# Kernel tuning notes

Measured on AMD Instinct MI355X. Metric: run time of the kernel, lower is better.

## Reference

```python
import jax, jax.numpy as jnp
import numpy as np

N, E, D, H = 50000, 500000, 128, 4
C = D // H
EPS = 1e-5


def _layer_norm(x, g, b):
    mu = jnp.mean(x, axis=-1, keepdims=True)
    var = jnp.mean((x - mu) ** 2, axis=-1, keepdims=True)
    return (x - mu) * jax.lax.rsqrt(var + EPS) * g + b


def setup_inputs() -> dict:
    key = jax.random.key(0)
    ks = jax.random.split(key, 20)
    f = lambda i, shape: jax.random.normal(ks[i], shape, dtype=jnp.float32) * 0.05
    return {
        "x": f(0, (N, D)),
        "edge_index": jax.random.randint(ks[1], (2, E), 0, N),
        "w_gcn": f(2, (D, D)), "b_gcn": f(3, (D,)),
        "wq": f(4, (D, D)), "bq": f(5, (D,)),
        "wk": f(6, (D, D)), "bk": f(7, (D,)),
        "wv": f(8, (D, D)), "bv": f(9, (D,)),
        "w_skip": f(10, (D, D)), "b_skip": f(11, (D,)),
        "w_beta": f(12, (3 * D, 1)),
        "g1": jnp.ones((D,), jnp.float32), "b1": jnp.zeros((D,), jnp.float32),
        "g2": jnp.ones((D,), jnp.float32), "b2": jnp.zeros((D,), jnp.float32),
        "w_rel": f(13, (D, 2 * D)), "w_root": f(14, (2 * D, D)),
        "local_w": jnp.ones((1,), jnp.float32), "global_w": jnp.ones((1,), jnp.float32),
    }


def reference(x, edge_index, w_gcn, b_gcn, wq, bq, wk, bk, wv, bv,
              w_skip, b_skip, w_beta, g1, b1, g2, b2, w_rel, w_root,
              local_w, global_w):
    src, dst = edge_index[0], edge_index[1]

    # ---- GCNConv (add_self_loops=False, symmetric norm) ----
    xw = x @ w_gcn                                   # [N, D]
    deg = jax.ops.segment_sum(jnp.ones((E,), x.dtype), dst, num_segments=N)
    dinv = jnp.where(deg > 0, jax.lax.rsqrt(jnp.maximum(deg, 1.0)), 0.0)
    coef = dinv[src] * dinv[dst]                     # [E]
    local_out = jax.ops.segment_sum(coef[:, None] * xw[src], dst, num_segments=N) + b_gcn

    # ---- TransformerConv (heads=4, concat=True, beta=True) ----
    q = (x @ wq + bq).reshape(N, H, C)
    k = (x @ wk + bk).reshape(N, H, C)
    v = (x @ wv + bv).reshape(N, H, C)
    alpha = jnp.sum(q[dst] * k[src], axis=-1) / jnp.sqrt(jnp.float32(C))  # [E, H]
    m = jax.ops.segment_max(alpha, dst, num_segments=N)
    m = jnp.where(jnp.isfinite(m), m, 0.0)
    a = jnp.exp(alpha - m[dst])
    s = jax.ops.segment_sum(a, dst, num_segments=N)
    attn = a / jnp.maximum(s[dst], 1e-16)            # [E, H] segment softmax over in-edges
    agg = jax.ops.segment_sum(attn[..., None] * v[src], dst, num_segments=N)
    out_g = agg.reshape(N, D)
    x_r = x @ w_skip + b_skip
    beta = jax.nn.sigmoid(jnp.concatenate([out_g, x_r, out_g - x_r], axis=-1) @ w_beta)
    global_out = beta * x_r + (1.0 - beta) * out_g

    # ---- combine + norm + FFN ----
    h = local_w * local_out + global_w * global_out
    h = _layer_norm(h + h, g1, b1)
    out = jax.nn.relu(h @ w_rel) @ w_root
    out = _layer_norm(out + h, g2, b2)
    return out
```

## Files before the change

### kernel.cpp

```cpp
#include <hip/hip_runtime.h>
#include <math.h>

#define D 128
#define EPSV 1e-5f

typedef unsigned short ushort_t;
typedef __attribute__((ext_vector_type(8))) short short8v;
typedef __attribute__((ext_vector_type(4))) float f32x4;

__device__ __forceinline__ float bf2f(unsigned u) {
    return __uint_as_float(u << 16);
}
__device__ __forceinline__ ushort_t f2bf(float f) {
    unsigned u = __float_as_uint(f);
    unsigned r = (u + 0x7fffu + ((u >> 16) & 1u)) >> 16;
    return (ushort_t)r;
}
__device__ __forceinline__ float bfp(uint4 v, int i) {
    unsigned w = (&v.x)[i >> 1];
    return bf2f((i & 1) ? (w >> 16) : (w & 0xffffu));
}

__global__ __launch_bounds__(256)
void proj_gemm(const float* __restrict__ x,
               const ushort_t* __restrict__ Bt,
               const float* __restrict__ bias,
               ushort_t* __restrict__ pack, ushort_t* __restrict__ qb,
               ushort_t* __restrict__ xrb, int M)
{
    __shared__ ushort_t Cs[128 * 136];
    const int tid = threadIdx.x, lane = tid & 63, wid = tid >> 6;
    const int wr = wid >> 1, wc = wid & 1;
    const int R0 = blockIdx.x * 128;
    const int cbeg = blockIdx.y ? 3 : 0;
    const int cend = blockIdx.y ? 5 : 3;

    short8v av[4][4];
    #pragma unroll
    for (int r = 0; r < 4; ++r) {
        int gr = R0 + wr * 64 + r * 16 + (lane & 15);
        if (gr >= M) gr = M - 1;
        const float* xrow = x + (size_t)gr * 128 + (lane >> 4) * 8;
        #pragma unroll
        for (int ks = 0; ks < 4; ++ks) {
            float4 lo = *reinterpret_cast<const float4*>(xrow + ks * 32);
            float4 hi = *reinterpret_cast<const float4*>(xrow + ks * 32 + 4);
            short8v a;
            a[0] = (short)f2bf(lo.x); a[1] = (short)f2bf(lo.y);
            a[2] = (short)f2bf(lo.z); a[3] = (short)f2bf(lo.w);
            a[4] = (short)f2bf(hi.x); a[5] = (short)f2bf(hi.y);
            a[6] = (short)f2bf(hi.z); a[7] = (short)f2bf(hi.w);
            av[r][ks] = a;
        }
    }

    for (int ct = cbeg; ct < cend; ++ct) {
        f32x4 acc[4][4] = {};
        #pragma unroll
        for (int ks = 0; ks < 4; ++ks) {
            short8v bv[4];
            #pragma unroll
            for (int c = 0; c < 4; ++c) {
                int col = ct * 128 + wc * 64 + c * 16 + (lane & 15);
                bv[c] = *reinterpret_cast<const short8v*>(
                    &Bt[(size_t)col * 128 + ks * 32 + (lane >> 4) * 8]);
            }
            #pragma unroll
            for (int r = 0; r < 4; ++r)
                #pragma unroll
                for (int c = 0; c < 4; ++c)
                    acc[r][c] = __builtin_amdgcn_mfma_f32_16x16x32_bf16(av[r][ks], bv[c], acc[r][c], 0, 0, 0);
        }
        __syncthreads();
        #pragma unroll
        for (int r = 0; r < 4; ++r) {
            int rowb = wr * 64 + r * 16 + (lane >> 4) * 4;
            #pragma unroll
            for (int i = 0; i < 4; ++i)
                #pragma unroll
                for (int c = 0; c < 4; ++c) {
                    int col = wc * 64 + c * 16 + (lane & 15);
                    Cs[(rowb + i) * 136 + col] = f2bf(acc[r][c][i] + bias[ct * 128 + col]);
                }
        }
        __syncthreads();
        #pragma unroll
        for (int it = 0; it < 8; ++it) {
            int linear = tid + it * 256;
            int row = linear >> 4, ch = linear & 15;
            int gr = R0 + row;
            if (gr < M) {
                uint4 v = *reinterpret_cast<const uint4*>(&Cs[row * 136 + ch * 8]);
                ushort_t* dst;
                if (ct == 0)      dst = pack + (size_t)gr * 384 + 256;
                else if (ct == 1) dst = qb   + (size_t)gr * 128;
                else if (ct == 2) dst = pack + (size_t)gr * 384;
                else if (ct == 3) dst = pack + (size_t)gr * 384 + 128;
                else              dst = xrb  + (size_t)gr * 128;
                *reinterpret_cast<uint4*>(dst + ch * 8) = v;
            }
        }
    }
}

__device__ __forceinline__ int swz(int ch, int row) {
    return (ch & 24) | ((ch ^ row) & 7);
}

__global__ __launch_bounds__(256)
void ffn_fused(const ushort_t* __restrict__ hlnb,
               const ushort_t* __restrict__ wt_rel,
               const ushort_t* __restrict__ wt_root,
               const float* __restrict__ g2, const float* __restrict__ b2,
               float* __restrict__ outf, int M)
{
    __shared__ float smem[128 * 130];
    ushort_t* Hs = (ushort_t*)smem;
    const int tid = threadIdx.x, lane = tid & 63, wid = tid >> 6;
    const int wr = wid >> 1, wc = wid & 1;
    const int R0 = blockIdx.x * 128;

    short8v av[4][4];
    #pragma unroll
    for (int r = 0; r < 4; ++r) {
        int gr = R0 + wr * 64 + r * 16 + (lane & 15);
        if (gr >= M) gr = M - 1;
        #pragma unroll
        for (int ks = 0; ks < 4; ++ks)
            av[r][ks] = *reinterpret_cast<const short8v*>(
                &hlnb[(size_t)gr * 128 + ks * 32 + (lane >> 4) * 8]);
    }
    for (int ct = 0; ct < 2; ++ct) {
        f32x4 acc[4][4] = {};
        #pragma unroll
        for (int ks = 0; ks < 4; ++ks) {
            short8v bv[4];
            #pragma unroll
            for (int c = 0; c < 4; ++c) {
                int col = ct * 128 + wc * 64 + c * 16 + (lane & 15);
                bv[c] = *reinterpret_cast<const short8v*>(
                    &wt_rel[(size_t)col * 128 + ks * 32 + (lane >> 4) * 8]);
            }
            #pragma unroll
            for (int r = 0; r < 4; ++r)
                #pragma unroll
                for (int c = 0; c < 4; ++c)
                    acc[r][c] = __builtin_amdgcn_mfma_f32_16x16x32_bf16(av[r][ks], bv[c], acc[r][c], 0, 0, 0);
        }
        #pragma unroll
        for (int r = 0; r < 4; ++r) {
            int rowb = wr * 64 + r * 16 + (lane >> 4) * 4;
            #pragma unroll
            for (int i = 0; i < 4; ++i)
                #pragma unroll
                for (int c = 0; c < 4; ++c) {
                    int row = rowb + i;
                    int col = ct * 128 + wc * 64 + c * 16 + (lane & 15);
                    int ch = col >> 3, el = col & 7;
                    Hs[row * 256 + swz(ch, row) * 8 + el] = f2bf(fmaxf(acc[r][c][i], 0.f));
                }
        }
    }
    __syncthreads();

    f32x4 acc2[4][4] = {};
    #pragma unroll
    for (int ks = 0; ks < 8; ++ks) {
        short8v a2[4], bv[4];
        #pragma unroll
        for (int r = 0; r < 4; ++r) {
            int row = wr * 64 + r * 16 + (lane & 15);
            int ch = ks * 4 + (lane >> 4);
            a2[r] = *reinterpret_cast<const short8v*>(&Hs[row * 256 + swz(ch, row) * 8]);
        }
        #pragma unroll
        for (int c = 0; c < 4; ++c) {
            int col = wc * 64 + c * 16 + (lane & 15);
            bv[c] = *reinterpret_cast<const short8v*>(
                &wt_root[(size_t)col * 256 + ks * 32 + (lane >> 4) * 8]);
        }
        #pragma unroll
        for (int r = 0; r < 4; ++r)
            #pragma unroll
            for (int c = 0; c < 4; ++c)
                acc2[r][c] = __builtin_amdgcn_mfma_f32_16x16x32_bf16(a2[r], bv[c], acc2[r][c], 0, 0, 0);
    }
    __syncthreads();

    float* Cs = smem;
    #pragma unroll
    for (int r = 0; r < 4; ++r) {
        int rowb = wr * 64 + r * 16 + (lane >> 4) * 4;
        #pragma unroll
        for (int i = 0; i < 4; ++i)
            #pragma unroll
            for (int c = 0; c < 4; ++c)
                Cs[(rowb + i) * 130 + wc * 64 + c * 16 + (lane & 15)] = acc2[r][c][i];
    }
    __syncthreads();

    const float ga = g2[lane * 2], gb = g2[lane * 2 + 1];
    const float ba = b2[lane * 2], bb2 = b2[lane * 2 + 1];
    for (int rr = 0; rr < 32; ++rr) {
        int row = wid * 32 + rr;
        int gr = R0 + row;
        if (gr >= M) break;
        unsigned hu = *reinterpret_cast<const unsigned*>(&hlnb[(size_t)gr * 128 + lane * 2]);
        float t0 = Cs[row * 130 + lane * 2]     + bf2f(hu & 0xffffu);
        float t1 = Cs[row * 130 + lane * 2 + 1] + bf2f(hu >> 16);
        float ssum = t0 + t1;
        #pragma unroll
        for (int off = 1; off <= 32; off <<= 1) ssum += __shfl_xor(ssum, off);
        float mu = ssum * (1.f / 128.f);
        float dv0 = t0 - mu, dv1 = t1 - mu;
        float vsum = dv0 * dv0 + dv1 * dv1;
        #pragma unroll
        for (int off = 1; off <= 32; off <<= 1) vsum += __shfl_xor(vsum, off);
        float rs = rsqrtf(vsum * (1.f / 128.f) + EPSV);
        float2 o = make_float2(dv0 * rs * ga + ba, dv1 * rs * gb + bb2);
        *reinterpret_cast<float2*>(&outf[(size_t)gr * 128 + lane * 2]) = o;
    }
}

__global__ void pack_weights_kernel(const float* __restrict__ wg, const float* __restrict__ wq,
                                    const float* __restrict__ wk, const float* __restrict__ wv,
                                    const float* __restrict__ wsk,
                                    const float* __restrict__ bq, const float* __restrict__ bk,
                                    const float* __restrict__ bv, const float* __restrict__ bsk,
                                    const float* __restrict__ wrel, const float* __restrict__ wroot,
                                    ushort_t* __restrict__ wt_all, ushort_t* __restrict__ wt_rel,
                                    ushort_t* __restrict__ wt_root, float* __restrict__ bias_all)
{
    int i = blockIdx.x * 256 + threadIdx.x;
    if (i < 640 * 128) {
        int n = i >> 7, k = i & 127;
        const float* srcs[5] = {wg, wq, wk, wv, wsk};
        wt_all[i] = f2bf(srcs[n >> 7][k * 128 + (n & 127)]);
    } else if (i < 640 * 128 + 256 * 128) {
        int j = i - 640 * 128;
        int n = j >> 7, k = j & 127;
        wt_rel[j] = f2bf(wrel[k * 256 + n]);
    } else if (i < 640 * 128 + 256 * 128 + 128 * 256) {
        int j = i - (640 * 128 + 256 * 128);
        int n = j >> 8, k = j & 255;
        wt_root[j] = f2bf(wroot[k * 128 + n]);
    } else if (i < 640 * 128 + 256 * 128 + 128 * 256 + 640) {
        int n = i - (640 * 128 + 256 * 128 + 128 * 256);
        float b = 0.f;
        if (n >= 128) {
            const float* bs[4] = {bq, bk, bv, bsk};
            b = bs[(n - 128) >> 7][n & 127];
        }
        bias_all[n] = b;
    }
}

__global__ void deg_count_kernel(const int* __restrict__ dst, int* __restrict__ deg, int E)
{
    int e = blockIdx.x * blockDim.x + threadIdx.x;
    if (e < E) atomicAdd(&deg[dst[e]], 1);
}

__global__ __launch_bounds__(256)
void scan1_kernel(const int* __restrict__ deg, int* __restrict__ row_start,
                  int* __restrict__ bsum, int n)
{
    __shared__ int ws[4];
    const int t = threadIdx.x, lane = t & 63, wid = t >> 6;
    const int base = blockIdx.x * 1024 + t * 4;
    int v0 = 0, v1 = 0, v2 = 0, v3 = 0;
    if (base + 3 < n) {
        int4 q = *reinterpret_cast<const int4*>(&deg[base]);
        v0 = q.x; v1 = q.y; v2 = q.z; v3 = q.w;
    } else {
        if (base < n)     v0 = deg[base];
        if (base + 1 < n) v1 = deg[base + 1];
        if (base + 2 < n) v2 = deg[base + 2];
        if (base + 3 < n) v3 = deg[base + 3];
    }
    int tot = v0 + v1 + v2 + v3;
    int inc = tot;
    #pragma unroll
    for (int off = 1; off < 64; off <<= 1) {
        int y = __shfl_up(inc, off);
        if (lane >= off) inc += y;
    }
    if (lane == 63) ws[wid] = inc;
    __syncthreads();
    int woff = 0;
    for (int w = 0; w < wid; ++w) woff += ws[w];
    int excl = woff + inc - tot;
    if (base < n)     row_start[base]     = excl;
    if (base + 1 < n) row_start[base + 1] = excl + v0;
    if (base + 2 < n) row_start[base + 2] = excl + v0 + v1;
    if (base + 3 < n) row_start[base + 3] = excl + v0 + v1 + v2;
    if (t == 0) bsum[blockIdx.x] = ws[0] + ws[1] + ws[2] + ws[3];
}

__global__ __launch_bounds__(256)
void scan2_kernel(int* __restrict__ bsum, int nb)
{
    __shared__ int ws[4];
    const int t = threadIdx.x, lane = t & 63, wid = t >> 6;
    const int base = t * 4;
    int v0 = 0, v1 = 0, v2 = 0, v3 = 0;
    if (base < nb)     v0 = bsum[base];
    if (base + 1 < nb) v1 = bsum[base + 1];
    if (base + 2 < nb) v2 = bsum[base + 2];
    if (base + 3 < nb) v3 = bsum[base + 3];
    int tot = v0 + v1 + v2 + v3;
    int inc = tot;
    #pragma unroll
    for (int off = 1; off < 64; off <<= 1) {
        int y = __shfl_up(inc, off);
        if (lane >= off) inc += y;
    }
    if (lane == 63) ws[wid] = inc;
    __syncthreads();
    int woff = 0;
    for (int w = 0; w < wid; ++w) woff += ws[w];
    int excl = woff + inc - tot;
    if (base < nb)     bsum[base]     = excl;
    if (base + 1 < nb) bsum[base + 1] = excl + v0;
    if (base + 2 < nb) bsum[base + 2] = excl + v0 + v1;
    if (base + 3 < nb) bsum[base + 3] = excl + v0 + v1 + v2;
}

__global__ void scan3_kernel(const int* __restrict__ deg, const int* __restrict__ bsum,
                             int* __restrict__ row_start, int* __restrict__ cursor,
                             float* __restrict__ dinv, int n, int E)
{
    int i = blockIdx.x * blockDim.x + threadIdx.x;
    if (i < n) {
        int rs = row_start[i] + bsum[i >> 10];
        row_start[i] = rs;
        cursor[i] = rs;
        int d = deg[i];
        dinv[i] = (d > 0) ? rsqrtf((float)d) : 0.f;
    }
    if (i == 0) row_start[n] = E;
}

__global__ void fill_kernel(const int* __restrict__ src, const int* __restrict__ dst,
                            int* __restrict__ cursor, int* __restrict__ csr_src, int E)
{
    int e = blockIdx.x * blockDim.x + threadIdx.x;
    if (e < E) {
        int d = dst[e];
        int pos = atomicAdd(&cursor[d], 1);
        csr_src[pos] = src[e];
    }
}

__global__ __launch_bounds__(256)
void edge_fused_kernel(const ushort_t* __restrict__ pack,
                       const ushort_t* __restrict__ qbf,
                       const ushort_t* __restrict__ xrbf,
                       const int* __restrict__ row_start,
                       const int* __restrict__ csr_src,
                       const float* __restrict__ dinv,
                       const float* __restrict__ b_gcn,
                       const float* __restrict__ w_beta,
                       const float* __restrict__ g1, const float* __restrict__ b1,
                       const float* __restrict__ local_w, const float* __restrict__ global_w,
                       ushort_t* __restrict__ hln_bf, int n)
{
    const int wid = threadIdx.x >> 6, lane = threadIdx.x & 63;
    const int node = blockIdx.x * 4 + wid;
    if (node >= n) return;
    const int slot = lane >> 4, li = lane & 15;
    const int d8 = li * 8;

    uint4 qu = *reinterpret_cast<const uint4*>(&qbf[(size_t)node * 128 + d8]);
    float q[8];
    #pragma unroll
    for (int i = 0; i < 8; ++i) q[i] = bfp(qu, i);

    const int e0 = row_start[node], e1 = row_start[node + 1];
    const float dn = dinv[node];
    const float scale = 0.17677669529663687f;

    float s = 0.f, va[8] = {}, ga[8] = {};

    for (int j = e0; j < e1; j += 4) {
        const int je = j + slot;
        const bool act = je < e1;
        const int sidx = act ? csr_src[je] : 0;
        const ushort_t* prow = pack + (size_t)sidx * 384;
        uint4 ku = *reinterpret_cast<const uint4*>(&prow[d8]);
        uint4 vu = *reinterpret_cast<const uint4*>(&prow[128 + d8]);
        uint4 xu = *reinterpret_cast<const uint4*>(&prow[256 + d8]);
        float p = 0.f;
        #pragma unroll
        for (int i = 0; i < 8; ++i) p = fmaf(q[i], bfp(ku, i), p);
        p += __shfl_xor(p, 1);
        p += __shfl_xor(p, 2);
        float wgt = act ? __expf(p * scale) : 0.f;
        float c   = act ? dn * dinv[sidx] : 0.f;
        s += wgt;
        #pragma unroll
        for (int i = 0; i < 8; ++i) {
            va[i] = fmaf(wgt, bfp(vu, i), va[i]);
            ga[i] = fmaf(c,   bfp(xu, i), ga[i]);
        }
    }
    #pragma unroll
    for (int off = 16; off <= 32; off <<= 1) {
        s += __shfl_xor(s, off);
        #pragma unroll
        for (int i = 0; i < 8; ++i) {
            va[i] += __shfl_xor(va[i], off);
            ga[i] += __shfl_xor(ga[i], off);
        }
    }
    const float denom = fmaxf(s, 1e-16f);

    uint4 xru = *reinterpret_cast<const uint4*>(&xrbf[(size_t)node * 128 + d8]);
    float t[8];
    float part = 0.f;
    #pragma unroll
    for (int i = 0; i < 8; ++i) {
        float og = va[i] / denom;
        float xr = bfp(xru, i);
        float lo = ga[i] + b_gcn[d8 + i];
        part += og * w_beta[d8 + i] + xr * w_beta[128 + d8 + i]
              + (og - xr) * w_beta[256 + d8 + i];
        t[i] = lo;
        va[i] = og; ga[i] = xr;
    }
    #pragma unroll
    for (int off = 1; off <= 32; off <<= 1) part += __shfl_xor(part, off);
    const float beta = 1.f / (1.f + __expf(-part * 0.25f));

    const float lw = local_w[0], gw = global_w[0];
    float ssum = 0.f;
    #pragma unroll
    for (int i = 0; i < 8; ++i) {
        float go = beta * ga[i] + (1.f - beta) * va[i];
        t[i] = 2.f * (lw * t[i] + gw * go);
        ssum += t[i];
    }
    #pragma unroll
    for (int off = 1; off <= 32; off <<= 1) ssum += __shfl_xor(ssum, off);
    const float mu = ssum * (1.f / 512.f);
    float vsum = 0.f;
    #pragma unroll
    for (int i = 0; i < 8; ++i) { float d = t[i] - mu; vsum += d * d; }
    #pragma unroll
    for (int off = 1; off <= 32; off <<= 1) vsum += __shfl_xor(vsum, off);
    const float rs = rsqrtf(vsum * (1.f / 512.f) + EPSV);

    if (slot == 0) {
        uint4 o;
        #pragma unroll
        for (int i = 0; i < 4; ++i) {
            float o0 = (t[2*i]   - mu) * rs * g1[d8 + 2*i]   + b1[d8 + 2*i];
            float o1 = (t[2*i+1] - mu) * rs * g1[d8 + 2*i+1] + b1[d8 + 2*i+1];
            (&o.x)[i] = (unsigned)f2bf(o0) | ((unsigned)f2bf(o1) << 16);
        }
        *reinterpret_cast<uint4*>(&hln_bf[(size_t)node * 128 + d8]) = o;
    }
}

extern "C" void kernel_launch(void* const* d_in, const int* in_sizes, int n_in,
                              void* d_out, int out_size, void* d_ws, size_t ws_size,
                              hipStream_t stream)
{
    const float* x      = (const float*)d_in[0];
    const int*   ei     = (const int*)d_in[1];
    const float* w_gcn  = (const float*)d_in[2];
    const float* b_gcn  = (const float*)d_in[3];
    const float* wq     = (const float*)d_in[4];
    const float* bq     = (const float*)d_in[5];
    const float* wk     = (const float*)d_in[6];
    const float* bk     = (const float*)d_in[7];
    const float* wv     = (const float*)d_in[8];
    const float* bv     = (const float*)d_in[9];
    const float* w_skip = (const float*)d_in[10];
    const float* b_skip = (const float*)d_in[11];
    const float* w_beta = (const float*)d_in[12];
    const float* g1     = (const float*)d_in[13];
    const float* b1     = (const float*)d_in[14];
    const float* g2     = (const float*)d_in[15];
    const float* b2     = (const float*)d_in[16];
    const float* w_rel  = (const float*)d_in[17];
    const float* w_root = (const float*)d_in[18];
    const float* lw     = (const float*)d_in[19];
    const float* gw     = (const float*)d_in[20];

    const int N = in_sizes[0] / D;
    const int E = in_sizes[1] / 2;
    const int* src = ei;
    const int* dst = ei + E;

    char* wsb = (char*)d_ws;
    size_t off = 0;
    auto alloc = [&](size_t bytes) -> void* {
        void* p = wsb + off;
        off += (bytes + 255) & ~(size_t)255;
        return p;
    };
    ushort_t* pack_kvx = (ushort_t*)alloc((size_t)N * 384 * 2);
    ushort_t* qb_bf    = (ushort_t*)alloc((size_t)N * 128 * 2);
    ushort_t* xr_bf    = (ushort_t*)alloc((size_t)N * 128 * 2);
    ushort_t* hln_bf   = (ushort_t*)alloc((size_t)N * 128 * 2);
    ushort_t* wt_all   = (ushort_t*)alloc(640 * 128 * 2);
    ushort_t* wt_rel   = (ushort_t*)alloc(256 * 128 * 2);
    ushort_t* wt_root  = (ushort_t*)alloc(128 * 256 * 2);
    float*    bias_all = (float*)alloc(640 * 4);
    int*      deg      = (int*)alloc((size_t)N * 4);
    int*      row_start= (int*)alloc((size_t)(N + 1) * 4);
    int*      cursor   = (int*)alloc((size_t)N * 4);
    int*      csr_src  = (int*)alloc((size_t)E * 4);
    float*    dinv     = (float*)alloc((size_t)N * 4);
    int*      bsum     = (int*)alloc(((size_t)(N + 1023) / 1024) * 4);

    float* out = (float*)d_out;
    const int SB = (N + 1023) / 1024;

    hipMemsetAsync(deg, 0, (size_t)N * sizeof(int), stream);
    deg_count_kernel<<<dim3((E + 255) / 256), dim3(256), 0, stream>>>(dst, deg, E);
    scan1_kernel<<<dim3(SB), dim3(256), 0, stream>>>(deg, row_start, bsum, N);
    scan2_kernel<<<dim3(1), dim3(256), 0, stream>>>(bsum, SB);
    scan3_kernel<<<dim3((N + 255) / 256), dim3(256), 0, stream>>>(
        deg, bsum, row_start, cursor, dinv, N, E);
    fill_kernel<<<dim3((E + 255) / 256), dim3(256), 0, stream>>>(src, dst, cursor, csr_src, E);

    pack_weights_kernel<<<dim3(579), dim3(256), 0, stream>>>(
        w_gcn, wq, wk, wv, w_skip, bq, bk, bv, b_skip, w_rel, w_root,
        wt_all, wt_rel, wt_root, bias_all);

    const int MB = (N + 127) / 128;
    proj_gemm<<<dim3(MB, 2), dim3(256), 0, stream>>>(
        x, wt_all, bias_all, pack_kvx, qb_bf, xr_bf, N);

    edge_fused_kernel<<<dim3((N + 3) / 4), dim3(256), 0, stream>>>(
        pack_kvx, qb_bf, xr_bf, row_start, csr_src, dinv, b_gcn, w_beta,
        g1, b1, lw, gw, hln_bf, N);

    ffn_fused<<<dim3(MB), dim3(256), 0, stream>>>(
        hln_bf, wt_rel, wt_root, g2, b2, out, N);
}
```

Before: 234.3 us.

## Fold key and value projections out of edge gather, aggregate raw features

The key weights are folded into the query side: each node gets a per-head q·Wk vector of 512 values. The key bias is dropped because it only shifts every logit of a destination node by the same amount, which cancels in the softmax. The edge kernel now gathers only bf16 x rows (128 values) instead of K, V and X rows (384 values). It builds per-head attention-weighted sums of x plus the GCN sum, and a new combine kernel applies Wv and Wgcn afterwards through MFMA GEMMs, then does the beta gate and the first LayerNorm. This cuts random gather bytes per edge, at the cost of more per-edge arithmetic and a large intermediate aggregate buffer that must be written and read back.

New measurement: 341.9 us. +45.9%, slower.

```diff
diff --git a/kernel.cpp b/kernel.cpp
--- a/kernel.cpp
+++ b/kernel.cpp
@@ -25,8 +25,10 @@
 void proj_gemm(const float* __restrict__ x,
                const ushort_t* __restrict__ Bt,
                const float* __restrict__ bias,
-               ushort_t* __restrict__ pack, ushort_t* __restrict__ qb,
-               ushort_t* __restrict__ xrb, int M)
+               ushort_t* __restrict__ qtb,
+               ushort_t* __restrict__ xrb,
+               ushort_t* __restrict__ xbf,
+               int M)
 {
     __shared__ ushort_t Cs[128 * 136];
     const int tid = threadIdx.x, lane = tid & 63, wid = tid >> 6;
@@ -54,6 +56,19 @@
         }
     }
 
+    if (blockIdx.y == 0) {
+        #pragma unroll
+        for (int r = 0; r < 4; ++r) {
+            int gr = R0 + wr * 64 + r * 16 + (lane & 15);
+            if (gr < M) {
+                #pragma unroll
+                for (int ks = 0; ks < 4; ++ks)
+                    *reinterpret_cast<short8v*>(
+                        &xbf[(size_t)gr * 128 + ks * 32 + (lane >> 4) * 8]) = av[r][ks];
+            }
+        }
+    }
+
     for (int ct = cbeg; ct < cend; ++ct) {
         f32x4 acc[4][4] = {};
         #pragma unroll
@@ -92,14 +107,247 @@
             if (gr < M) {
                 uint4 v = *reinterpret_cast<const uint4*>(&Cs[row * 136 + ch * 8]);
                 ushort_t* dst;
-                if (ct == 0)      dst = pack + (size_t)gr * 384 + 256;
-                else if (ct == 1) dst = qb   + (size_t)gr * 128;
-                else if (ct == 2) dst = pack + (size_t)gr * 384;
-                else if (ct == 3) dst = pack + (size_t)gr * 384 + 128;
-                else              dst = xrb  + (size_t)gr * 128;
+                if (ct < 4) dst = qtb + (size_t)gr * 512 + ct * 128;
+                else        dst = xrb + (size_t)gr * 128;
                 *reinterpret_cast<uint4*>(dst + ch * 8) = v;
             }
         }
+    }
+}
+
+__global__ __launch_bounds__(256)
+void edge_fused_kernel(const ushort_t* __restrict__ xbf,
+                       const ushort_t* __restrict__ qtb,
+                       const int* __restrict__ row_start,
+                       const int* __restrict__ csr_src,
+                       const float* __restrict__ dinv,
+                       ushort_t* __restrict__ agg,
+                       float* __restrict__ flag,
+                       int n)
+{
+    const int wid = threadIdx.x >> 6, lane = threadIdx.x & 63;
+    const int node = blockIdx.x * 4 + wid;
+    if (node >= n) return;
+    const int slot = lane >> 4, li = lane & 15;
+    const int d8 = li * 8;
+
+    float qf[4][8];
+    #pragma unroll
+    for (int h = 0; h < 4; ++h) {
+        uint4 qu = *reinterpret_cast<const uint4*>(&qtb[(size_t)node * 512 + h * 128 + d8]);
+        #pragma unroll
+        for (int i = 0; i < 8; ++i) qf[h][i] = bfp(qu, i);
+    }
+
+    const int e0 = row_start[node], e1 = row_start[node + 1];
+    const float dn = dinv[node];
+    const float scale = 0.17677669529663687f;
+
+    float sh[4] = {}, va[4][8] = {}, ga[8] = {};
+
+    for (int j = e0; j < e1; j += 4) {
+        const int je = j + slot;
+        const bool act = je < e1;
+        const int sidx = act ? csr_src[je] : 0;
+        uint4 xu = *reinterpret_cast<const uint4*>(&xbf[(size_t)sidx * 128 + d8]);
+        float xv[8];
+        #pragma unroll
+        for (int i = 0; i < 8; ++i) xv[i] = bfp(xu, i);
+        float p[4];
+        #pragma unroll
+        for (int h = 0; h < 4; ++h) {
+            float t = 0.f;
+            #pragma unroll
+            for (int i = 0; i < 8; ++i) t = fmaf(qf[h][i], xv[i], t);
+            t += __shfl_xor(t, 1);
+            t += __shfl_xor(t, 2);
+            t += __shfl_xor(t, 4);
+            t += __shfl_xor(t, 8);
+            p[h] = t;
+        }
+        const float c = act ? dn * dinv[sidx] : 0.f;
+        #pragma unroll
+        for (int h = 0; h < 4; ++h) {
+            float w = act ? __expf(p[h] * scale) : 0.f;
+            sh[h] += w;
+            #pragma unroll
+            for (int i = 0; i < 8; ++i) va[h][i] = fmaf(w, xv[i], va[h][i]);
+        }
+        #pragma unroll
+        for (int i = 0; i < 8; ++i) ga[i] = fmaf(c, xv[i], ga[i]);
+    }
+    #pragma unroll
+    for (int off = 16; off <= 32; off <<= 1) {
+        #pragma unroll
+        for (int h = 0; h < 4; ++h) {
+            sh[h] += __shfl_xor(sh[h], off);
+            #pragma unroll
+            for (int i = 0; i < 8; ++i) va[h][i] += __shfl_xor(va[h][i], off);
+        }
+        #pragma unroll
+        for (int i = 0; i < 8; ++i) ga[i] += __shfl_xor(ga[i], off);
+    }
+
+    if (slot == 0) {
+        #pragma unroll
+        for (int h = 0; h < 4; ++h) {
+            float r = 1.f / fmaxf(sh[h], 1e-16f);
+            uint4 o;
+            #pragma unroll
+            for (int i = 0; i < 4; ++i)
+                (&o.x)[i] = (unsigned)f2bf(va[h][2 * i] * r)
+                          | ((unsigned)f2bf(va[h][2 * i + 1] * r) << 16);
+            *reinterpret_cast<uint4*>(&agg[(size_t)node * 640 + h * 128 + d8]) = o;
+        }
+        uint4 og;
+        #pragma unroll
+        for (int i = 0; i < 4; ++i)
+            (&og.x)[i] = (unsigned)f2bf(ga[2 * i]) | ((unsigned)f2bf(ga[2 * i + 1]) << 16);
+        *reinterpret_cast<uint4*>(&agg[(size_t)node * 640 + 512 + d8]) = og;
+        if (li == 0) flag[node] = (sh[0] > 0.f) ? 1.f : 0.f;
+    }
+}
+
+__global__ __launch_bounds__(256)
+void combine_ln1(const ushort_t* __restrict__ agg,
+                 const ushort_t* __restrict__ wt_vg,
+                 const float* __restrict__ bvv, const float* __restrict__ b_gcn,
+                 const float* __restrict__ flag,
+                 const ushort_t* __restrict__ xrb,
+                 const float* __restrict__ w_beta,
+                 const float* __restrict__ g1, const float* __restrict__ b1,
+                 const float* __restrict__ local_w, const float* __restrict__ global_w,
+                 ushort_t* __restrict__ hln_bf, int M)
+{
+    __shared__ float OgS[128 * 130];
+    __shared__ float LoS[128 * 130];
+    const int tid = threadIdx.x, lane = tid & 63, wid = tid >> 6;
+    const int wr = wid >> 1, wc = wid & 1;
+    const int R0 = blockIdx.x * 128;
+
+    {
+        f32x4 acc[4][4] = {};
+        #pragma unroll
+        for (int hl = 0; hl < 2; ++hl) {
+            const int head = wc * 2 + hl;
+            short8v av[4][4];
+            #pragma unroll
+            for (int r = 0; r < 4; ++r) {
+                int gr = R0 + wr * 64 + r * 16 + (lane & 15);
+                if (gr >= M) gr = M - 1;
+                #pragma unroll
+                for (int ks = 0; ks < 4; ++ks)
+                    av[r][ks] = *reinterpret_cast<const short8v*>(
+                        &agg[(size_t)gr * 640 + head * 128 + ks * 32 + (lane >> 4) * 8]);
+            }
+            #pragma unroll
+            for (int cfl = 0; cfl < 2; ++cfl) {
+                const int cf = hl * 2 + cfl;
+                const int col = wc * 64 + cf * 16 + (lane & 15);
+                #pragma unroll
+                for (int ks = 0; ks < 4; ++ks) {
+                    short8v bfrag = *reinterpret_cast<const short8v*>(
+                        &wt_vg[(size_t)col * 128 + ks * 32 + (lane >> 4) * 8]);
+                    #pragma unroll
+                    for (int r = 0; r < 4; ++r)
+                        acc[r][cf] = __builtin_amdgcn_mfma_f32_16x16x32_bf16(av[r][ks], bfrag, acc[r][cf], 0, 0, 0);
+                }
+            }
+        }
+        #pragma unroll
+        for (int r = 0; r < 4; ++r) {
+            int rowb = wr * 64 + r * 16 + (lane >> 4) * 4;
+            #pragma unroll
+            for (int i = 0; i < 4; ++i)
+                #pragma unroll
+                for (int cf = 0; cf < 4; ++cf)
+                    OgS[(rowb + i) * 130 + wc * 64 + cf * 16 + (lane & 15)] = acc[r][cf][i];
+        }
+    }
+    {
+        f32x4 acc[4][4] = {};
+        short8v av[4][4];
+        #pragma unroll
+        for (int r = 0; r < 4; ++r) {
+            int gr = R0 + wr * 64 + r * 16 + (lane & 15);
+            if (gr >= M) gr = M - 1;
+            #pragma unroll
+            for (int ks = 0; ks < 4; ++ks)
+                av[r][ks] = *reinterpret_cast<const short8v*>(
+                    &agg[(size_t)gr * 640 + 512 + ks * 32 + (lane >> 4) * 8]);
+        }
+        #pragma unroll
+        for (int ks = 0; ks < 4; ++ks) {
+            short8v bfrag[4];
+            #pragma unroll
+            for (int cf = 0; cf < 4; ++cf) {
+                int col = wc * 64 + cf * 16 + (lane & 15);
+                bfrag[cf] = *reinterpret_cast<const short8v*>(
+                    &wt_vg[(size_t)(128 + col) * 128 + ks * 32 + (lane >> 4) * 8]);
+            }
+            #pragma unroll
+            for (int r = 0; r < 4; ++r)
+                #pragma unroll
+                for (int cf = 0; cf < 4; ++cf)
+                    acc[r][cf] = __builtin_amdgcn_mfma_f32_16x16x32_bf16(av[r][ks], bfrag[cf], acc[r][cf], 0, 0, 0);
+        }
+        #pragma unroll
+        for (int r = 0; r < 4; ++r) {
+            int rowb = wr * 64 + r * 16 + (lane >> 4) * 4;
+            #pragma unroll
+            for (int i = 0; i < 4; ++i)
+                #pragma unroll
+                for (int cf = 0; cf < 4; ++cf)
+                    LoS[(rowb + i) * 130 + wc * 64 + cf * 16 + (lane & 15)] = acc[r][cf][i];
+        }
+    }
+    __syncthreads();
+
+    const int d0 = lane * 2, d1 = d0 + 1;
+    const float lw = local_w[0], gw = global_w[0];
+    const float bv0 = bvv[d0], bv1 = bvv[d1];
+    const float bg0 = b_gcn[d0], bg1 = b_gcn[d1];
+    const float wb00 = w_beta[d0],       wb01 = w_beta[d1];
+    const float wb10 = w_beta[128 + d0], wb11 = w_beta[128 + d1];
+    const float wb20 = w_beta[256 + d0], wb21 = w_beta[256 + d1];
+    const float g1a = g1[d0], g1b = g1[d1], b1a = b1[d0], b1b = b1[d1];
+
+    for (int rr = 0; rr < 32; ++rr) {
+        int row = wid * 32 + rr;
+        int gr = R0 + row;
+        if (gr >= M) break;
+        const float fl = flag[gr];
+        float og0 = OgS[row * 130 + d0] + fl * bv0;
+        float og1 = OgS[row * 130 + d1] + fl * bv1;
+        float lo0 = LoS[row * 130 + d0] + bg0;
+        float lo1 = LoS[row * 130 + d1] + bg1;
+        unsigned xu = *reinterpret_cast<const unsigned*>(&xrb[(size_t)gr * 128 + d0]);
+        float xr0 = bf2f(xu & 0xffffu), xr1 = bf2f(xu >> 16);
+
+        float part = og0 * wb00 + og1 * wb01 + xr0 * wb10 + xr1 * wb11
+                   + (og0 - xr0) * wb20 + (og1 - xr1) * wb21;
+        #pragma unroll
+        for (int off = 1; off <= 32; off <<= 1) part += __shfl_xor(part, off);
+        const float beta = 1.f / (1.f + __expf(-part));
+
+        float go0 = beta * xr0 + (1.f - beta) * og0;
+        float go1 = beta * xr1 + (1.f - beta) * og1;
+        float t0 = 2.f * (lw * lo0 + gw * go0);
+        float t1 = 2.f * (lw * lo1 + gw * go1);
+
+        float ssum = t0 + t1;
+        #pragma unroll
+        for (int off = 1; off <= 32; off <<= 1) ssum += __shfl_xor(ssum, off);
+        float mu = ssum * (1.f / 128.f);
+        float dv0 = t0 - mu, dv1 = t1 - mu;
+        float vsum = dv0 * dv0 + dv1 * dv1;
+        #pragma unroll
+        for (int off = 1; off <= 32; off <<= 1) vsum += __shfl_xor(vsum, off);
+        float rs = rsqrtf(vsum * (1.f / 128.f) + EPSV);
+        float o0 = dv0 * rs * g1a + b1a;
+        float o1 = dv1 * rs * g1b + b1b;
+        *reinterpret_cast<unsigned*>(&hln_bf[(size_t)gr * 128 + d0]) =
+            (unsigned)f2bf(o0) | ((unsigned)f2bf(o1) << 16);
     }
 }
 
@@ -225,33 +473,53 @@
 __global__ void pack_weights_kernel(const float* __restrict__ wg, const float* __restrict__ wq,
                                     const float* __restrict__ wk, const float* __restrict__ wv,
                                     const float* __restrict__ wsk,
-                                    const float* __restrict__ bq, const float* __restrict__ bk,
-                                    const float* __restrict__ bv, const float* __restrict__ bsk,
+                                    const float* __restrict__ bq, const float* __restrict__ bsk,
                                     const float* __restrict__ wrel, const float* __restrict__ wroot,
-                                    ushort_t* __restrict__ wt_all, ushort_t* __restrict__ wt_rel,
-                                    ushort_t* __restrict__ wt_root, float* __restrict__ bias_all)
+                                    ushort_t* __restrict__ wt_all, ushort_t* __restrict__ wt_vg,
+                                    ushort_t* __restrict__ wt_rel, ushort_t* __restrict__ wt_root,
+                                    float* __restrict__ bias_all)
 {
     int i = blockIdx.x * 256 + threadIdx.x;
     if (i < 640 * 128) {
-        int n = i >> 7, k = i & 127;
-        const float* srcs[5] = {wg, wq, wk, wv, wsk};
-        wt_all[i] = f2bf(srcs[n >> 7][k * 128 + (n & 127)]);
-    } else if (i < 640 * 128 + 256 * 128) {
-        int j = i - 640 * 128;
-        int n = j >> 7, k = j & 127;
-        wt_rel[j] = f2bf(wrel[k * 256 + n]);
-    } else if (i < 640 * 128 + 256 * 128 + 128 * 256) {
-        int j = i - (640 * 128 + 256 * 128);
-        int n = j >> 8, k = j & 255;
-        wt_root[j] = f2bf(wroot[k * 128 + n]);
-    } else if (i < 640 * 128 + 256 * 128 + 128 * 256 + 640) {
-        int n = i - (640 * 128 + 256 * 128 + 128 * 256);
-        float b = 0.f;
-        if (n >= 128) {
-            const float* bs[4] = {bq, bk, bv, bsk};
-            b = bs[(n - 128) >> 7][n & 127];
-        }
-        bias_all[n] = b;
+        int c = i >> 7, k = i & 127;
+        float v;
+        if (c < 512) {
+            int h = c >> 7, d = c & 127;
+            float acc = 0.f;
+            #pragma unroll
+            for (int j = 0; j < 32; ++j)
+                acc = fmaf(wq[k * 128 + h * 32 + j], wk[d * 128 + h * 32 + j], acc);
+            v = acc;
+        } else {
+            v = wsk[k * 128 + (c - 512)];
+        }
+        wt_all[i] = f2bf(v);
+    } else if (i < 640 * 128 + 640) {
+        int c = i - 640 * 128;
+        float b;
+        if (c < 512) {
+            int h = c >> 7, d = c & 127;
+            float acc = 0.f;
+            #pragma unroll
+            for (int j = 0; j < 32; ++j)
+                acc = fmaf(bq[h * 32 + j], wk[d * 128 + h * 32 + j], acc);
+            b = acc;
+        } else {
+            b = bsk[c - 512];
+        }
+        bias_all[c] = b;
+    } else if (i < 640 * 128 + 640 + 256 * 128) {
+        int j = i - (640 * 128 + 640);
+        int c = j >> 7, k = j & 127;
+        wt_vg[j] = f2bf(c < 128 ? wv[k * 128 + c] : wg[k * 128 + (c - 128)]);
+    } else if (i < 640 * 128 + 640 + 2 * 256 * 128) {
+        int j = i - (640 * 128 + 640 + 256 * 128);
+        int c = j >> 7, k = j & 127;
+        wt_rel[j] = f2bf(wrel[k * 256 + c]);
+    } else if (i < 640 * 128 + 640 + 2 * 256 * 128 + 128 * 256) {
+        int j = i - (640 * 128 + 640 + 2 * 256 * 128);
+        int c = j >> 8, k = j & 255;
+        wt_root[j] = f2bf(wroot[k * 128 + c]);
     }
 }
 
@@ -349,116 +617,6 @@
         int d = dst[e];
         int pos = atomicAdd(&cursor[d], 1);
         csr_src[pos] = src[e];
-    }
-}
-
-__global__ __launch_bounds__(256)
-void edge_fused_kernel(const ushort_t* __restrict__ pack,
-                       const ushort_t* __restrict__ qbf,
-                       const ushort_t* __restrict__ xrbf,
-                       const int* __restrict__ row_start,
-                       const int* __restrict__ csr_src,
-                       const float* __restrict__ dinv,
-                       const float* __restrict__ b_gcn,
-                       const float* __restrict__ w_beta,
-                       const float* __restrict__ g1, const float* __restrict__ b1,
-                       const float* __restrict__ local_w, const float* __restrict__ global_w,
-                       ushort_t* __restrict__ hln_bf, int n)
-{
-    const int wid = threadIdx.x >> 6, lane = threadIdx.x & 63;
-    const int node = blockIdx.x * 4 + wid;
-    if (node >= n) return;
-    const int slot = lane >> 4, li = lane & 15;
-    const int d8 = li * 8;
-
-    uint4 qu = *reinterpret_cast<const uint4*>(&qbf[(size_t)node * 128 + d8]);
-    float q[8];
-    #pragma unroll
-    for (int i = 0; i < 8; ++i) q[i] = bfp(qu, i);
-
-    const int e0 = row_start[node], e1 = row_start[node + 1];
-    const float dn = dinv[node];
-    const float scale = 0.17677669529663687f;
-
-    float s = 0.f, va[8] = {}, ga[8] = {};
-
-    for (int j = e0; j < e1; j += 4) {
-        const int je = j + slot;
-        const bool act = je < e1;
-        const int sidx = act ? csr_src[je] : 0;
-        const ushort_t* prow = pack + (size_t)sidx * 384;
-        uint4 ku = *reinterpret_cast<const uint4*>(&prow[d8]);
-        uint4 vu = *reinterpret_cast<const uint4*>(&prow[128 + d8]);
-        uint4 xu = *reinterpret_cast<const uint4*>(&prow[256 + d8]);
-        float p = 0.f;
-        #pragma unroll
-        for (int i = 0; i < 8; ++i) p = fmaf(q[i], bfp(ku, i), p);
-        p += __shfl_xor(p, 1);
-        p += __shfl_xor(p, 2);
-        float wgt = act ? __expf(p * scale) : 0.f;
-        float c   = act ? dn * dinv[sidx] : 0.f;
-        s += wgt;
-        #pragma unroll
-        for (int i = 0; i < 8; ++i) {
-            va[i] = fmaf(wgt, bfp(vu, i), va[i]);
-            ga[i] = fmaf(c,   bfp(xu, i), ga[i]);
-        }
-    }
-    #pragma unroll
-    for (int off = 16; off <= 32; off <<= 1) {
-        s += __shfl_xor(s, off);
-        #pragma unroll
-        for (int i = 0; i < 8; ++i) {
-            va[i] += __shfl_xor(va[i], off);
-            ga[i] += __shfl_xor(ga[i], off);
-        }
-    }
-    const float denom = fmaxf(s, 1e-16f);
-
-    uint4 xru = *reinterpret_cast<const uint4*>(&xrbf[(size_t)node * 128 + d8]);
-    float t[8];
-    float part = 0.f;
-    #pragma unroll
-    for (int i = 0; i < 8; ++i) {
-        float og = va[i] / denom;
-        float xr = bfp(xru, i);
-        float lo = ga[i] + b_gcn[d8 + i];
-        part += og * w_beta[d8 + i] + xr * w_beta[128 + d8 + i]
-              + (og - xr) * w_beta[256 + d8 + i];
-        t[i] = lo;
-        va[i] = og; ga[i] = xr;
-    }
-    #pragma unroll
-    for (int off = 1; off <= 32; off <<= 1) part += __shfl_xor(part, off);
-    const float beta = 1.f / (1.f + __expf(-part * 0.25f));
-
-    const float lw = local_w[0], gw = global_w[0];
-    float ssum = 0.f;
-    #pragma unroll
-    for (int i = 0; i < 8; ++i) {
-        float go = beta * ga[i] + (1.f - beta) * va[i];
-        t[i] = 2.f * (lw * t[i] + gw * go);
-        ssum += t[i];
-    }
-    #pragma unroll
-    for (int off = 1; off <= 32; off <<= 1) ssum += __shfl_xor(ssum, off);
-    const float mu = ssum * (1.f / 512.f);
-    float vsum = 0.f;
-    #pragma unroll
-    for (int i = 0; i < 8; ++i) { float d = t[i] - mu; vsum += d * d; }
-    #pragma unroll
-    for (int off = 1; off <= 32; off <<= 1) vsum += __shfl_xor(vsum, off);
-    const float rs = rsqrtf(vsum * (1.f / 512.f) + EPSV);
-
-    if (slot == 0) {
-        uint4 o;
-        #pragma unroll
-        for (int i = 0; i < 4; ++i) {
-            float o0 = (t[2*i]   - mu) * rs * g1[d8 + 2*i]   + b1[d8 + 2*i];
-            float o1 = (t[2*i+1] - mu) * rs * g1[d8 + 2*i+1] + b1[d8 + 2*i+1];
-            (&o.x)[i] = (unsigned)f2bf(o0) | ((unsigned)f2bf(o1) << 16);
-        }
-        *reinterpret_cast<uint4*>(&hln_bf[(size_t)node * 128 + d8]) = o;
     }
 }
 
@@ -487,6 +645,7 @@
     const float* w_root = (const float*)d_in[18];
     const float* lw     = (const float*)d_in[19];
     const float* gw     = (const float*)d_in[20];
+    (void)bk;
 
     const int N = in_sizes[0] / D;
     const int E = in_sizes[1] / 2;
@@ -500,11 +659,14 @@
         off += (bytes + 255) & ~(size_t)255;
         return p;
     };
-    ushort_t* pack_kvx = (ushort_t*)alloc((size_t)N * 384 * 2);
-    ushort_t* qb_bf    = (ushort_t*)alloc((size_t)N * 128 * 2);
+    ushort_t* qtb      = (ushort_t*)alloc((size_t)N * 512 * 2);
+    ushort_t* xbf      = (ushort_t*)alloc((size_t)N * 128 * 2);
     ushort_t* xr_bf    = (ushort_t*)alloc((size_t)N * 128 * 2);
+    ushort_t* agg      = (ushort_t*)alloc((size_t)N * 640 * 2);
+    float*    flagb    = (float*)alloc((size_t)N * 4);
     ushort_t* hln_bf   = (ushort_t*)alloc((size_t)N * 128 * 2);
     ushort_t* wt_all   = (ushort_t*)alloc(640 * 128 * 2);
+    ushort_t* wt_vg    = (ushort_t*)alloc(256 * 128 * 2);
     ushort_t* wt_rel   = (ushort_t*)alloc(256 * 128 * 2);
     ushort_t* wt_root  = (ushort_t*)alloc(128 * 256 * 2);
     float*    bias_all = (float*)alloc(640 * 4);
@@ -526,17 +688,20 @@
         deg, bsum, row_start, cursor, dinv, N, E);
     fill_kernel<<<dim3((E + 255) / 256), dim3(256), 0, stream>>>(src, dst, cursor, csr_src, E);
 
-    pack_weights_kernel<<<dim3(579), dim3(256), 0, stream>>>(
-        w_gcn, wq, wk, wv, w_skip, bq, bk, bv, b_skip, w_rel, w_root,
-        wt_all, wt_rel, wt_root, bias_all);
+    const int PW = (640 * 128 + 640 + 2 * 256 * 128 + 128 * 256 + 255) / 256;
+    pack_weights_kernel<<<dim3(PW), dim3(256), 0, stream>>>(
+        w_gcn, wq, wk, wv, w_skip, bq, b_skip, w_rel, w_root,
+        wt_all, wt_vg, wt_rel, wt_root, bias_all);
 
     const int MB = (N + 127) / 128;
     proj_gemm<<<dim3(MB, 2), dim3(256), 0, stream>>>(
-        x, wt_all, bias_all, pack_kvx, qb_bf, xr_bf, N);
+        x, wt_all, bias_all, qtb, xr_bf, xbf, N);
 
     edge_fused_kernel<<<dim3((N + 3) / 4), dim3(256), 0, stream>>>(
-        pack_kvx, qb_bf, xr_bf, row_start, csr_src, dinv, b_gcn, w_beta,
-        g1, b1, lw, gw, hln_bf, N);
+        xbf, qtb, row_start, csr_src, dinv, agg, flagb, N);
+
+    combine_ln1<<<dim3(MB), dim3(256), 0, stream>>>(
+        agg, wt_vg, bv, b_gcn, flagb, xr_bf, w_beta, g1, b1, lw, gw, hln_bf, N);
 
     ffn_fused<<<dim3(MB), dim3(256), 0, stream>>>(
         hln_bf, wt_rel, wt_root, g2, b2, out, N);
```

## Store gathered K/V/XW rows in fp8 and fold scan2 into scan3

Applied to the files above, without the earlier changes.

The projection GEMM now writes the K, V and GCN-weighted X columns as fp8 (e4m3) instead of bf16, halving the per-edge gather bytes in the edge-fused kernel, which unpacks them with hardware cvt_pk_f32_fp8. Separately, the single-block scan2 launch is removed and each scan3 block sums the preceding block totals serially in thread 0. The fp8 storage cuts memory traffic in the gather-bound edge pass but loses precision, which risks tolerance failures. The scan change saves a launch at the cost of a small serial loop.

New measurement: 215.1 us. 1.09x faster.

```diff
diff --git a/kernel.cpp b/kernel.cpp
--- a/kernel.cpp
+++ b/kernel.cpp
@@ -5,8 +5,10 @@
 #define EPSV 1e-5f
 
 typedef unsigned short ushort_t;
+typedef unsigned char uchar_t;
 typedef __attribute__((ext_vector_type(8))) short short8v;
 typedef __attribute__((ext_vector_type(4))) float f32x4;
+typedef __attribute__((ext_vector_type(2))) float f32x2;
 
 __device__ __forceinline__ float bf2f(unsigned u) {
     return __uint_as_float(u << 16);
@@ -21,11 +23,25 @@
     return bf2f((i & 1) ? (w >> 16) : (w & 0xffffu));
 }
 
+#define UNPACK8_FP8(u, o) { \
+    f32x2 _a = __builtin_amdgcn_cvt_pk_f32_fp8((int)(u).x, false); \
+    f32x2 _b = __builtin_amdgcn_cvt_pk_f32_fp8((int)(u).x, true);  \
+    f32x2 _c = __builtin_amdgcn_cvt_pk_f32_fp8((int)(u).y, false); \
+    f32x2 _d = __builtin_amdgcn_cvt_pk_f32_fp8((int)(u).y, true);  \
+    o[0] = _a.x; o[1] = _a.y; o[2] = _b.x; o[3] = _b.y;            \
+    o[4] = _c.x; o[5] = _c.y; o[6] = _d.x; o[7] = _d.y; }
+
+__device__ __forceinline__ unsigned bf4_to_fp8x4(unsigned w0, unsigned w1) {
+    int u = __builtin_amdgcn_cvt_pk_fp8_f32(bf2f(w0 & 0xffffu), bf2f(w0 >> 16), 0, false);
+    u = __builtin_amdgcn_cvt_pk_fp8_f32(bf2f(w1 & 0xffffu), bf2f(w1 >> 16), u, true);
+    return (unsigned)u;
+}
+
 __global__ __launch_bounds__(256)
 void proj_gemm(const float* __restrict__ x,
                const ushort_t* __restrict__ Bt,
                const float* __restrict__ bias,
-               ushort_t* __restrict__ pack, ushort_t* __restrict__ qb,
+               uchar_t* __restrict__ pack, ushort_t* __restrict__ qb,
                ushort_t* __restrict__ xrb, int M)
 {
     __shared__ ushort_t Cs[128 * 136];
@@ -84,20 +100,36 @@
                 }
         }
         __syncthreads();
-        #pragma unroll
-        for (int it = 0; it < 8; ++it) {
-            int linear = tid + it * 256;
-            int row = linear >> 4, ch = linear & 15;
-            int gr = R0 + row;
-            if (gr < M) {
-                uint4 v = *reinterpret_cast<const uint4*>(&Cs[row * 136 + ch * 8]);
-                ushort_t* dst;
-                if (ct == 0)      dst = pack + (size_t)gr * 384 + 256;
-                else if (ct == 1) dst = qb   + (size_t)gr * 128;
-                else if (ct == 2) dst = pack + (size_t)gr * 384;
-                else if (ct == 3) dst = pack + (size_t)gr * 384 + 128;
-                else              dst = xrb  + (size_t)gr * 128;
-                *reinterpret_cast<uint4*>(dst + ch * 8) = v;
+        if (ct == 1 || ct == 4) {
+            #pragma unroll
+            for (int it = 0; it < 8; ++it) {
+                int linear = tid + it * 256;
+                int row = linear >> 4, ch = linear & 15;
+                int gr = R0 + row;
+                if (gr < M) {
+                    uint4 v = *reinterpret_cast<const uint4*>(&Cs[row * 136 + ch * 8]);
+                    ushort_t* dst = (ct == 1) ? (qb + (size_t)gr * 128)
+                                              : (xrb + (size_t)gr * 128);
+                    *reinterpret_cast<uint4*>(dst + ch * 8) = v;
+                }
+            }
+        } else {
+            const int byteoff = (ct == 0) ? 256 : (ct == 2) ? 0 : 128;
+            #pragma unroll
+            for (int it = 0; it < 4; ++it) {
+                int linear = tid + it * 256;
+                int row = linear >> 3, ch = linear & 7;
+                int gr = R0 + row;
+                if (gr < M) {
+                    uint4 lo = *reinterpret_cast<const uint4*>(&Cs[row * 136 + ch * 16]);
+                    uint4 hi = *reinterpret_cast<const uint4*>(&Cs[row * 136 + ch * 16 + 8]);
+                    uint4 o;
+                    o.x = bf4_to_fp8x4(lo.x, lo.y);
+                    o.y = bf4_to_fp8x4(lo.z, lo.w);
+                    o.z = bf4_to_fp8x4(hi.x, hi.y);
+                    o.w = bf4_to_fp8x4(hi.z, hi.w);
+                    *reinterpret_cast<uint4*>(pack + (size_t)gr * 384 + byteoff + ch * 16) = o;
+                }
             }
         }
     }
@@ -298,41 +330,21 @@
 }
 
 __global__ __launch_bounds__(256)
-void scan2_kernel(int* __restrict__ bsum, int nb)
-{
-    __shared__ int ws[4];
-    const int t = threadIdx.x, lane = t & 63, wid = t >> 6;
-    const int base = t * 4;
-    int v0 = 0, v1 = 0, v2 = 0, v3 = 0;
-    if (base < nb)     v0 = bsum[base];
-    if (base + 1 < nb) v1 = bsum[base + 1];
-    if (base + 2 < nb) v2 = bsum[base + 2];
-    if (base + 3 < nb) v3 = bsum[base + 3];
-    int tot = v0 + v1 + v2 + v3;
-    int inc = tot;
-    #pragma unroll
-    for (int off = 1; off < 64; off <<= 1) {
-        int y = __shfl_up(inc, off);
-        if (lane >= off) inc += y;
-    }
-    if (lane == 63) ws[wid] = inc;
+void scan3_kernel(const int* __restrict__ deg, const int* __restrict__ bsum,
+                  int* __restrict__ row_start, int* __restrict__ cursor,
+                  float* __restrict__ dinv, int n, int E)
+{
+    __shared__ int boff_s;
+    const int K = blockIdx.x >> 2;
+    if (threadIdx.x == 0) {
+        int s = 0;
+        for (int j = 0; j < K; ++j) s += bsum[j];
+        boff_s = s;
+    }
     __syncthreads();
-    int woff = 0;
-    for (int w = 0; w < wid; ++w) woff += ws[w];
-    int excl = woff + inc - tot;
-    if (base < nb)     bsum[base]     = excl;
-    if (base + 1 < nb) bsum[base + 1] = excl + v0;
-    if (base + 2 < nb) bsum[base + 2] = excl + v0 + v1;
-    if (base + 3 < nb) bsum[base + 3] = excl + v0 + v1 + v2;
-}
-
-__global__ void scan3_kernel(const int* __restrict__ deg, const int* __restrict__ bsum,
-                             int* __restrict__ row_start, int* __restrict__ cursor,
-                             float* __restrict__ dinv, int n, int E)
-{
-    int i = blockIdx.x * blockDim.x + threadIdx.x;
+    int i = blockIdx.x * 256 + threadIdx.x;
     if (i < n) {
-        int rs = row_start[i] + bsum[i >> 10];
+        int rs = row_start[i] + boff_s;
         row_start[i] = rs;
         cursor[i] = rs;
         int d = deg[i];
@@ -353,7 +365,7 @@
 }
 
 __global__ __launch_bounds__(256)
-void edge_fused_kernel(const ushort_t* __restrict__ pack,
+void edge_fused_kernel(const uchar_t* __restrict__ pack,
                        const ushort_t* __restrict__ qbf,
                        const ushort_t* __restrict__ xrbf,
                        const int* __restrict__ row_start,
@@ -386,13 +398,17 @@
         const int je = j + slot;
         const bool act = je < e1;
         const int sidx = act ? csr_src[je] : 0;
-        const ushort_t* prow = pack + (size_t)sidx * 384;
-        uint4 ku = *reinterpret_cast<const uint4*>(&prow[d8]);
-        uint4 vu = *reinterpret_cast<const uint4*>(&prow[128 + d8]);
-        uint4 xu = *reinterpret_cast<const uint4*>(&prow[256 + d8]);
+        const uchar_t* prow = pack + (size_t)sidx * 384;
+        uint2 ku = *reinterpret_cast<const uint2*>(prow + d8);
+        uint2 vu = *reinterpret_cast<const uint2*>(prow + 128 + d8);
+        uint2 xu = *reinterpret_cast<const uint2*>(prow + 256 + d8);
+        float kf[8], vf[8], xf[8];
+        UNPACK8_FP8(ku, kf);
+        UNPACK8_FP8(vu, vf);
+        UNPACK8_FP8(xu, xf);
         float p = 0.f;
         #pragma unroll
-        for (int i = 0; i < 8; ++i) p = fmaf(q[i], bfp(ku, i), p);
+        for (int i = 0; i < 8; ++i) p = fmaf(q[i], kf[i], p);
         p += __shfl_xor(p, 1);
         p += __shfl_xor(p, 2);
         float wgt = act ? __expf(p * scale) : 0.f;
@@ -400,8 +416,8 @@
         s += wgt;
         #pragma unroll
         for (int i = 0; i < 8; ++i) {
-            va[i] = fmaf(wgt, bfp(vu, i), va[i]);
-            ga[i] = fmaf(c,   bfp(xu, i), ga[i]);
+            va[i] = fmaf(wgt, vf[i], va[i]);
+            ga[i] = fmaf(c,   xf[i], ga[i]);
         }
     }
     #pragma unroll
@@ -500,7 +516,7 @@
         off += (bytes + 255) & ~(size_t)255;
         return p;
     };
-    ushort_t* pack_kvx = (ushort_t*)alloc((size_t)N * 384 * 2);
+    uchar_t*  pack_kvx = (uchar_t*)alloc((size_t)N * 384);
     ushort_t* qb_bf    = (ushort_t*)alloc((size_t)N * 128 * 2);
     ushort_t* xr_bf    = (ushort_t*)alloc((size_t)N * 128 * 2);
     ushort_t* hln_bf   = (ushort_t*)alloc((size_t)N * 128 * 2);
@@ -521,7 +537,6 @@
     hipMemsetAsync(deg, 0, (size_t)N * sizeof(int), stream);
     deg_count_kernel<<<dim3((E + 255) / 256), dim3(256), 0, stream>>>(dst, deg, E);
     scan1_kernel<<<dim3(SB), dim3(256), 0, stream>>>(deg, row_start, bsum, N);
-    scan2_kernel<<<dim3(1), dim3(256), 0, stream>>>(bsum, SB);
     scan3_kernel<<<dim3((N + 255) / 256), dim3(256), 0, stream>>>(
         deg, bsum, row_start, cursor, dinv, N, E);
     fill_kernel<<<dim3((E + 255) / 256), dim3(256), 0, stream>>>(src, dst, cursor, csr_src, E);
```
